# Performance work log

Measured on AMD Instinct MI355X. Metric: run time of the kernel, lower is better.

The kernel has to match this reference:

```python
import jax, jax.numpy as jnp
import numpy as np

THRESHOLD = 0.5
NEG_POS_RATIO = 3
ALPHA = 10.0
N_PRIORS = 8732
N_CLASSES = 21
BATCH = 128
N_OBJ = 32


def cxcy_to_xy(cxcy):
    return jnp.concatenate([cxcy[..., :2] - cxcy[..., 2:] / 2.0,
                            cxcy[..., :2] + cxcy[..., 2:] / 2.0], axis=-1)


def xy_to_cxcy(xy):
    return jnp.concatenate([(xy[..., :2] + xy[..., 2:]) / 2.0,
                            xy[..., 2:] - xy[..., :2]], axis=-1)


def cxcy_to_gcxgcy(cxcy, priors_cxcy):
    return jnp.concatenate([(cxcy[..., :2] - priors_cxcy[..., :2]) / (priors_cxcy[..., 2:] / 10.0),
                            jnp.log(cxcy[..., 2:] / priors_cxcy[..., 2:]) * 5.0], axis=-1)


def find_jaccard_overlap(a, b):
    # a: (M,4) xyxy, b: (P,4) xyxy -> (M,P)
    lt = jnp.maximum(a[:, None, :2], b[None, :, :2])
    rb = jnp.minimum(a[:, None, 2:], b[None, :, 2:])
    wh = jnp.clip(rb - lt, 0.0)
    inter = wh[..., 0] * wh[..., 1]
    area_a = (a[:, 2] - a[:, 0]) * (a[:, 3] - a[:, 1])
    area_b = (b[:, 2] - b[:, 0]) * (b[:, 3] - b[:, 1])
    return inter / (area_a[:, None] + area_b[None, :] - inter)


def _match_one(boxes, labels, priors_xy, priors_cxcy):
    # boxes: (M,4) xyxy, labels: (M,)
    iou = find_jaccard_overlap(boxes, priors_xy)           # (M,P)
    obj_idx = jnp.argmax(iou, axis=1)                      # best prior per object
    iou = iou.at[jnp.arange(boxes.shape[0]), obj_idx].set(1.0)
    positive = (iou >= THRESHOLD).any(axis=0)              # (P,)
    max_prior_idx = jnp.argmax(iou, axis=0)                # best object per prior
    true_cls = labels[max_prior_idx] * positive.astype(labels.dtype)
    matched = boxes[max_prior_idx]                         # (P,4)
    true_locs = cxcy_to_gcxgcy(xy_to_cxcy(matched), priors_cxcy)
    return true_locs, true_cls, positive


def setup_inputs() -> dict:
    key = jax.random.key(0)
    k1, k2, k3, k4, k5, k6 = jax.random.split(key, 6)
    pred_loc = jax.random.normal(k1, (BATCH, N_PRIORS, 4), dtype=jnp.float32)
    pred_cls = jax.random.normal(k2, (BATCH, N_PRIORS, N_CLASSES), dtype=jnp.float32)
    # valid xyxy gt boxes in [0,1]
    p1 = jax.random.uniform(k3, (BATCH, N_OBJ, 2))
    p2 = jax.random.uniform(k4, (BATCH, N_OBJ, 2))
    b_boxes = jnp.concatenate([jnp.minimum(p1, p2), jnp.maximum(p1, p2) + 1e-3], axis=-1)
    b_boxes = jnp.clip(b_boxes, 0.0, 1.0).astype(jnp.float32)
    b_labels = jax.random.randint(k5, (BATCH, N_OBJ), 1, N_CLASSES)
    cxy = jax.random.uniform(k6, (N_PRIORS, 2), minval=0.1, maxval=0.9)
    wh = jax.random.uniform(jax.random.fold_in(k6, 1), (N_PRIORS, 2), minval=0.05, maxval=0.3)
    priors_cxcy = jnp.concatenate([cxy, wh], axis=-1).astype(jnp.float32)
    return {"pred_loc": pred_loc, "pred_cls": pred_cls, "b_boxes": b_boxes,
            "b_labels": b_labels, "priors_cxcy": priors_cxcy}


def reference(pred_loc, pred_cls, b_boxes, b_labels, priors_cxcy):
    batch_size, n_priors, n_classes = pred_cls.shape
    priors_xy = cxcy_to_xy(priors_cxcy)
    true_locs, true_classes, positive = jax.vmap(
        _match_one, in_axes=(0, 0, None, None))(b_boxes, b_labels, priors_xy, priors_cxcy)
    pos_f = positive.astype(pred_loc.dtype)                 # (B,P)
    n_positives = positive.sum(axis=1)                      # (B,)
    n_pos_total = n_positives.sum().astype(pred_loc.dtype)
    # L1 loss (mean over positive box elements)
    loc_loss = (jnp.abs(pred_loc - true_locs) * pos_f[..., None]).sum() / (n_pos_total * 4.0)
    # per-prior cross-entropy
    logp = jax.nn.log_softmax(pred_cls, axis=-1)
    ce = -jnp.take_along_axis(logp, true_classes[..., None], axis=-1)[..., 0]  # (B,P)
    conf_loss_pos = (ce * pos_f).sum()
    # hard negative mining: sort negatives descending per image
    conf_neg = jnp.where(positive, 0.0, ce)
    conf_neg_sorted = -jnp.sort(-conf_neg, axis=1)
    ranks = jnp.arange(n_priors)[None, :]
    hard_mask = ranks < (NEG_POS_RATIO * n_positives)[:, None]
    conf_loss_hard_neg = jnp.where(hard_mask, conf_neg_sorted, 0.0).sum()
    conf_loss = (conf_loss_hard_neg + conf_loss_pos) / n_pos_total
    loc_loss = ALPHA * loc_loss
    total_loss = conf_loss + loc_loss
    return total_loss, loc_loss, conf_loss
```

## Files before the change

### kernel.cpp

```cpp
#include <hip/hip_runtime.h>
#include <math.h>

#define B 128
#define M 32
#define P 8732
#define C 21
#define ALPHA 10.0f
#define TPB2 256
#define PPT 2
#define PPB (TPB2 * PPT)
#define NB2 18
#define CH 8
#define CS 1092

__global__ __launch_bounds__(256) void k1_partial(
    const float* __restrict__ b_boxes, const float* __restrict__ priors,
    float* __restrict__ pI, float* __restrict__ pU, int* __restrict__ pidx,
    int* __restrict__ done) {
  if (blockIdx.x == 0 && threadIdx.x == 0) *done = 0;
  int b = blockIdx.x >> 3;
  int ch = blockIdx.x & 7;
  int wid = threadIdx.x >> 6;
  int lane = threadIdx.x & 63;
  int obase = wid * 8;

  float ox1[8], oy1[8], ox2[8], oy2[8], oarea[8], bI[8], bU[8];
  int bidx[8];
#pragma unroll
  for (int k = 0; k < 8; k++) {
    float4 bx = ((const float4*)b_boxes)[(size_t)b * M + obase + k];
    ox1[k] = bx.x; oy1[k] = bx.y; ox2[k] = bx.z; oy2[k] = bx.w;
    oarea[k] = (bx.z - bx.x) * (bx.w - bx.y);
    bI[k] = -1.0f; bU[k] = 1.0f; bidx[k] = P;
  }

  int pend = (ch + 1) * CS;
  if (pend > P) pend = P;
#pragma unroll 2
  for (int p = ch * CS + lane; p < pend; p += 64) {
    float4 pr = ((const float4*)priors)[p];
    float pw2 = pr.z * 0.5f, ph2 = pr.w * 0.5f;
    float px1 = pr.x - pw2, py1 = pr.y - ph2;
    float px2 = pr.x + pw2, py2 = pr.y + ph2;
    float areaP = pr.z * pr.w;
#pragma unroll
    for (int k = 0; k < 8; k++) {
      float iw = fminf(ox2[k], px2) - fmaxf(ox1[k], px1);
      float ih = fminf(oy2[k], py2) - fmaxf(oy1[k], py1);
      iw = fmaxf(iw, 0.0f);
      ih = fmaxf(ih, 0.0f);
      float inter = iw * ih;
      float uni = oarea[k] + areaP - inter;
      if (inter * bU[k] > bI[k] * uni) { bI[k] = inter; bU[k] = uni; bidx[k] = p; }
    }
  }
  for (int off = 32; off >= 1; off >>= 1) {
#pragma unroll
    for (int k = 0; k < 8; k++) {
      float oI = __shfl_xor(bI[k], off, 64);
      float oU = __shfl_xor(bU[k], off, 64);
      int oi = __shfl_xor(bidx[k], off, 64);
      float l = oI * bU[k], r = bI[k] * oU;
      if (l > r || (l == r && oi < bidx[k])) { bI[k] = oI; bU[k] = oU; bidx[k] = oi; }
    }
  }
  if (lane == 0) {
#pragma unroll
    for (int k = 0; k < 8; k++) {
      int idx = ((size_t)b * M + obase + k) * CH + ch;
      pI[idx] = bI[k]; pU[idx] = bU[k]; pidx[idx] = bidx[k];
    }
  }
}

__global__ __launch_bounds__(256) void k1_reduce(
    const float* __restrict__ pI, const float* __restrict__ pU,
    const int* __restrict__ pidx, int* __restrict__ objidx) {
  int o = blockIdx.x * 256 + threadIdx.x;
  if (o >= B * M) return;
  float cI = pI[o * CH], cU = pU[o * CH];
  int ci = pidx[o * CH];
#pragma unroll
  for (int ch = 1; ch < CH; ch++) {
    float nI = pI[o * CH + ch], nU = pU[o * CH + ch];
    int ni = pidx[o * CH + ch];
    if (nI * cU > cI * nU) { cI = nI; cU = nU; ci = ni; }
  }
  objidx[o] = ci;
}

__global__ __launch_bounds__(TPB2, 5) void k2_perprior(
    const float* __restrict__ pred_loc, const float* __restrict__ pred_cls,
    const float* __restrict__ b_boxes, const int* __restrict__ b_labels,
    const float* __restrict__ priors, const int* __restrict__ objidx,
    float* __restrict__ ploc, float* __restrict__ pce, int* __restrict__ pnp,
    float* __restrict__ confneg) {
  int b = blockIdx.y;
  int p0 = blockIdx.x * PPB;
  int tid = threadIdx.x;

  __shared__ float sx1[M], sy1[M], sx2[M], sy2[M], sarea[M];
  __shared__ int slab[M], sobj[M];
  __shared__ int sinv[PPB];
  if (tid < M) {
    int m = tid;
    float4 bx = ((const float4*)b_boxes)[b * M + m];
    sx1[m] = bx.x; sy1[m] = bx.y; sx2[m] = bx.z; sy2[m] = bx.w;
    sarea[m] = (bx.z - bx.x) * (bx.w - bx.y);
    slab[m] = b_labels[b * M + m];
    sobj[m] = objidx[b * M + m];
  }
  sinv[tid] = 0x7fffffff;
  sinv[tid + 256] = 0x7fffffff;
  __syncthreads();
  if (tid < M) {
    int t = sobj[tid] - p0;
    if (t >= 0 && t < PPB) atomicMin(&sinv[t], tid);
  }
  __syncthreads();

  float locpart = 0.0f, cepospart = 0.0f;
  int npos = 0;
  int pbase = p0 + tid * PPT;
  if (pbase < P) {
    float4 pr[PPT];
    pr[0] = ((const float4*)priors)[pbase];
    pr[1] = ((const float4*)priors)[pbase + 1];
    const float2* pc2 =
        (const float2*)(pred_cls + ((size_t)b * P + p0) * C) + 21 * tid;
    float2 q[21];
#pragma unroll
    for (int i = 0; i < 21; i++) q[i] = pc2[i];
    const float* u = (const float*)q;
    const float4* plp = (const float4*)pred_loc + (size_t)b * P + pbase;
    float4 pl[PPT];
    pl[0] = plp[0];
    pl[1] = plp[1];

    float px1[PPT], py1[PPT], px2[PPT], py2[PPT], areaP[PPT];
    float bI[PPT], bU[PPT];
    int bm[PPT];
#pragma unroll
    for (int j = 0; j < PPT; j++) {
      float pw2 = pr[j].z * 0.5f, ph2 = pr[j].w * 0.5f;
      px1[j] = pr[j].x - pw2; py1[j] = pr[j].y - ph2;
      px2[j] = pr[j].x + pw2; py2[j] = pr[j].y + ph2;
      areaP[j] = pr[j].z * pr[j].w;
      bI[j] = -1.0f; bU[j] = 1.0f; bm[j] = 0;
    }
    for (int m = 0; m < M; m++) {
      float bx1 = sx1[m], by1 = sy1[m], bx2 = sx2[m], by2 = sy2[m];
      float ar = sarea[m];
#pragma unroll
      for (int j = 0; j < PPT; j++) {
        float iw = fminf(bx2, px2[j]) - fmaxf(bx1, px1[j]);
        float ih = fminf(by2, py2[j]) - fmaxf(by1, py1[j]);
        iw = fmaxf(iw, 0.0f);
        ih = fmaxf(ih, 0.0f);
        float inter = iw * ih;
        float uni = ar + areaP[j] - inter;
        if (inter * bU[j] > bI[j] * uni) { bI[j] = inter; bU[j] = uni; bm[j] = m; }
      }
    }
    bool pos[PPT];
#pragma unroll
    for (int j = 0; j < PPT; j++) {
      int fm = sinv[tid * PPT + j];
      if (fm != 0x7fffffff) {
        if (!((bI[j] == bU[j]) && (bm[j] < fm))) {
          bI[j] = 1.0f; bU[j] = 1.0f; bm[j] = fm;
        }
      }
      pos[j] = (2.0f * bI[j] >= bU[j]);
    }
    int wAny = __any((int)(pos[0] | pos[1]));

    if (wAny) {
#pragma unroll
      for (int j = 0; j < PPT; j++) {
        int mj = bm[j];
        float bx1 = sx1[mj], by1 = sy1[mj], bx2 = sx2[mj], by2 = sy2[mj];
        float cx = (bx1 + bx2) * 0.5f, cy = (by1 + by2) * 0.5f;
        float w = bx2 - bx1, h = by2 - by1;
        float rz = __builtin_amdgcn_rcpf(pr[j].z);
        float rw = __builtin_amdgcn_rcpf(pr[j].w);
        float g0 = (cx - pr[j].x) * 10.0f * rz;
        float g1 = (cy - pr[j].y) * 10.0f * rw;
        float g2 = __logf(w * rz) * 5.0f;
        float g3 = __logf(h * rw) * 5.0f;
        if (pos[j]) {
          locpart += fabsf(pl[j].x - g0) + fabsf(pl[j].y - g1) +
                     fabsf(pl[j].z - g2) + fabsf(pl[j].w - g3);
          npos++;
        }
      }
    }

    float cn[PPT];
#pragma unroll
    for (int j = 0; j < PPT; j++) {
      float se = 0.0f;
#pragma unroll
      for (int c = 0; c < C; c++) se += __expf(u[j * C + c]);
      float lse = __logf(se);
      cn[j] = pos[j] ? 0.0f : (lse - u[j * C]);
      if (wAny) {
        int cls = pos[j] ? slab[bm[j]] : 0;
        float vc = u[j * C];
#pragma unroll
        for (int c = 1; c < C; c++)
          if (c == cls) vc = u[j * C + c];
        cepospart += pos[j] ? (lse - vc) : 0.0f;
      }
    }
    ((float2*)confneg)[((size_t)b * P + pbase) >> 1] = make_float2(cn[0], cn[1]);
  }

  for (int off = 32; off >= 1; off >>= 1) {
    locpart += __shfl_down(locpart, off, 64);
    cepospart += __shfl_down(cepospart, off, 64);
    npos += __shfl_down(npos, off, 64);
  }
  __shared__ float rloc[4], rce[4];
  __shared__ int rnp[4];
  int wid = tid >> 6;
  if ((tid & 63) == 0) { rloc[wid] = locpart; rce[wid] = cepospart; rnp[wid] = npos; }
  __syncthreads();
  if (tid == 0) {
    int f = b * NB2 + blockIdx.x;
    ploc[f] = rloc[0] + rloc[1] + rloc[2] + rloc[3];
    pce[f] = rce[0] + rce[1] + rce[2] + rce[3];
    pnp[f] = rnp[0] + rnp[1] + rnp[2] + rnp[3];
  }
}

__global__ __launch_bounds__(1024) void k3_hardneg(
    const float* __restrict__ confneg,
    const float* __restrict__ ploc, const float* __restrict__ pce,
    const int* __restrict__ pnp,
    float* __restrict__ imgres, int* __restrict__ done,
    float* __restrict__ out) {
  int b = blockIdx.x;
  int tid = threadIdx.x;
  int wid = tid >> 6;
  int lane = tid & 63;

  __shared__ __align__(16) float s[P];
  __shared__ int histw[16 * 256];
  __shared__ __align__(16) int cnt[256];
  __shared__ int sdig, scum, sK, sLast;
  __shared__ float sLoc, sCe, sNp;
  __shared__ float rsum[16], rl[16], rc[16], rh[16], rn[16];
  __shared__ int rcnt[16];

  {
    const float4* row4 = (const float4*)(confneg + (size_t)b * P);
    for (int i = tid; i < P / 4; i += 1024) ((float4*)s)[i] = row4[i];
  }

  if (wid == 0) {
    float lp = 0.0f, cp = 0.0f;
    int np = 0;
    if (lane < NB2) {
      int f = b * NB2 + lane;
      lp = ploc[f]; cp = pce[f]; np = pnp[f];
    }
    for (int off = 32; off >= 1; off >>= 1) {
      lp += __shfl_down(lp, off, 64);
      cp += __shfl_down(cp, off, 64);
      np += __shfl_down(np, off, 64);
    }
    if (lane == 0) {
      int K = np * 3;
      if (K > P) K = P;
      sK = K; sLoc = lp; sCe = cp; sNp = (float)np;
    }
  }
  __syncthreads();

  int K = sK;
  unsigned pfx = 0;
  int Krem = K;
#pragma unroll
  for (int pass = 3; pass >= 0; --pass) {
    int sh = pass * 8;
    for (int i = tid; i < 16 * 256; i += 1024) histw[i] = 0;
    __syncthreads();
    unsigned himask = (pass == 3) ? 0u : (0xFFFFFFFFu << (sh + 8));
    int* myh = &histw[wid * 256];
    for (int i = tid; i < P; i += 1024) {
      unsigned ub = __float_as_uint(s[i]);
      if ((ub & himask) == pfx) atomicAdd(&myh[(ub >> sh) & 255], 1);
    }
    __syncthreads();
    if (tid < 256) {
      int c = 0;
#pragma unroll
      for (int w = 0; w < 16; w++) c += histw[w * 256 + tid];
      cnt[tid] = c;
    }
    __syncthreads();
    if (wid == 0) {
      int4 c4 = ((const int4*)cnt)[lane];
      int s3 = c4.w;
      int s2 = c4.z + s3;
      int s1 = c4.y + s2;
      int s0 = c4.x + s1;
      int suf = s0;
      for (int off = 1; off < 64; off <<= 1) {
        int t = __shfl_down(suf, off, 64);
        if (lane + off < 64) suf += t;
      }
      int above = suf - s0;
      int S0 = above + s0, S1 = above + s1, S2 = above + s2, S3 = above + s3;
      int S4 = above;
      if (S3 >= Krem && S4 < Krem) { sdig = 4 * lane + 3; scum = S4; }
      else if (S2 >= Krem && S3 < Krem) { sdig = 4 * lane + 2; scum = S3; }
      else if (S1 >= Krem && S2 < Krem) { sdig = 4 * lane + 1; scum = S2; }
      else if (S0 >= Krem && S1 < Krem) { sdig = 4 * lane + 0; scum = S1; }
    }
    __syncthreads();
    pfx |= ((unsigned)sdig) << sh;
    Krem -= scum;
  }
  float tau = __uint_as_float(pfx);

  float sum = 0.0f;
  int cgt = 0;
  for (int i = tid; i < P; i += 1024) {
    float v = s[i];
    if (v > tau) { sum += v; cgt++; }
  }
  for (int off = 32; off >= 1; off >>= 1) {
    sum += __shfl_down(sum, off, 64);
    cgt += __shfl_down(cgt, off, 64);
  }
  if (lane == 0) { rsum[wid] = sum; rcnt[wid] = cgt; }
  __syncthreads();
  if (tid == 0) {
    float stot = 0.0f;
    int ctot = 0;
#pragma unroll
    for (int w = 0; w < 16; w++) { stot += rsum[w]; ctot += rcnt[w]; }
    float hard = stot + (float)(K - ctot) * tau;
    imgres[b * 4 + 0] = sLoc;
    imgres[b * 4 + 1] = sCe;
    imgres[b * 4 + 2] = hard;
    imgres[b * 4 + 3] = sNp;
    __threadfence();
    int prev = atomicAdd(done, 1);
    sLast = (prev == B - 1) ? 1 : 0;
  }
  __syncthreads();
  if (sLast) {
    __threadfence();
    float l = 0.0f, c = 0.0f, h = 0.0f, n = 0.0f;
    if (tid < B) {
      l = atomicAdd(&imgres[tid * 4 + 0], 0.0f);
      c = atomicAdd(&imgres[tid * 4 + 1], 0.0f);
      h = atomicAdd(&imgres[tid * 4 + 2], 0.0f);
      n = atomicAdd(&imgres[tid * 4 + 3], 0.0f);
    }
    for (int off = 32; off >= 1; off >>= 1) {
      l += __shfl_down(l, off, 64);
      c += __shfl_down(c, off, 64);
      h += __shfl_down(h, off, 64);
      n += __shfl_down(n, off, 64);
    }
    if (lane == 0) { rl[wid] = l; rc[wid] = c; rh[wid] = h; rn[wid] = n; }
    __syncthreads();
    if (tid == 0) {
      float L = 0, Cc = 0, H = 0, N = 0;
#pragma unroll
      for (int w = 0; w < 16; w++) { L += rl[w]; Cc += rc[w]; H += rh[w]; N += rn[w]; }
      float loc = ALPHA * L / (N * 4.0f);
      float conf = (H + Cc) / N;
      out[0] = conf + loc;
      out[1] = loc;
      out[2] = conf;
    }
  }
}

extern "C" void kernel_launch(void* const* d_in, const int* in_sizes, int n_in,
                              void* d_out, int out_size, void* d_ws, size_t ws_size,
                              hipStream_t stream) {
  (void)in_sizes; (void)n_in; (void)out_size; (void)ws_size;
  const float* pred_loc = (const float*)d_in[0];
  const float* pred_cls = (const float*)d_in[1];
  const float* b_boxes = (const float*)d_in[2];
  const int* b_labels = (const int*)d_in[3];
  const float* priors = (const float*)d_in[4];
  float* out = (float*)d_out;

  int* done = (int*)d_ws;
  float* ploc = (float*)d_ws + 8;
  float* pce = ploc + B * NB2;
  int* pnp = (int*)(pce + B * NB2);
  float* imgres = (float*)(pnp + B * NB2);
  float* pI = imgres + B * 4;
  float* pU = pI + B * M * CH;
  int* pidx = (int*)(pU + B * M * CH);
  int* objidx = pidx + B * M * CH;
  float* confneg = (float*)(objidx + B * M);

  k1_partial<<<B * CH, 256, 0, stream>>>(b_boxes, priors, pI, pU, pidx, done);
  k1_reduce<<<(B * M + 255) / 256, 256, 0, stream>>>(pI, pU, pidx, objidx);
  dim3 g2(NB2, B);
  k2_perprior<<<g2, TPB2, 0, stream>>>(pred_loc, pred_cls, b_boxes, b_labels,
                                       priors, objidx, ploc, pce, pnp, confneg);
  k3_hardneg<<<B, 1024, 0, stream>>>(confneg, ploc, pce, pnp, imgres, done, out);
}
```

Baseline: 221.6 us.

## Fold objidx reduction into per-prior kernel and stage class logits through LDS

```diff
diff --git a/kernel.cpp b/kernel.cpp
--- a/kernel.cpp
+++ b/kernel.cpp
@@ -7,9 +7,8 @@
 #define C 21
 #define ALPHA 10.0f
 #define TPB2 256
-#define PPT 2
-#define PPB (TPB2 * PPT)
-#define NB2 18
+#define PPB 256
+#define NB2 35
 #define CH 8
 #define CS 1092
 
@@ -73,147 +72,117 @@
   }
 }
 
-__global__ __launch_bounds__(256) void k1_reduce(
-    const float* __restrict__ pI, const float* __restrict__ pU,
-    const int* __restrict__ pidx, int* __restrict__ objidx) {
-  int o = blockIdx.x * 256 + threadIdx.x;
-  if (o >= B * M) return;
-  float cI = pI[o * CH], cU = pU[o * CH];
-  int ci = pidx[o * CH];
-#pragma unroll
-  for (int ch = 1; ch < CH; ch++) {
-    float nI = pI[o * CH + ch], nU = pU[o * CH + ch];
-    int ni = pidx[o * CH + ch];
-    if (nI * cU > cI * nU) { cI = nI; cU = nU; ci = ni; }
-  }
-  objidx[o] = ci;
-}
-
-__global__ __launch_bounds__(TPB2, 5) void k2_perprior(
+__global__ __launch_bounds__(TPB2) void k2_perprior(
     const float* __restrict__ pred_loc, const float* __restrict__ pred_cls,
     const float* __restrict__ b_boxes, const int* __restrict__ b_labels,
-    const float* __restrict__ priors, const int* __restrict__ objidx,
+    const float* __restrict__ priors,
+    const float* __restrict__ pI, const float* __restrict__ pU,
+    const int* __restrict__ pidx,
     float* __restrict__ ploc, float* __restrict__ pce, int* __restrict__ pnp,
     float* __restrict__ confneg) {
   int b = blockIdx.y;
   int p0 = blockIdx.x * PPB;
   int tid = threadIdx.x;
-
+  int wid = tid >> 6;
+  int lane = tid & 63;
+
+  __shared__ __align__(16) float sCls[4 * 64 * C];
   __shared__ float sx1[M], sy1[M], sx2[M], sy2[M], sarea[M];
   __shared__ int slab[M], sobj[M];
   __shared__ int sinv[PPB];
+
+  sinv[tid] = 0x7fffffff;
   if (tid < M) {
     int m = tid;
     float4 bx = ((const float4*)b_boxes)[b * M + m];
     sx1[m] = bx.x; sy1[m] = bx.y; sx2[m] = bx.z; sy2[m] = bx.w;
     sarea[m] = (bx.z - bx.x) * (bx.w - bx.y);
     slab[m] = b_labels[b * M + m];
-    sobj[m] = objidx[b * M + m];
-  }
-  sinv[tid] = 0x7fffffff;
-  sinv[tid + 256] = 0x7fffffff;
+    int o = b * M + m;
+    float cI = pI[o * CH], cU = pU[o * CH];
+    int ci = pidx[o * CH];
+#pragma unroll
+    for (int ch = 1; ch < CH; ch++) {
+      float nI = pI[o * CH + ch], nU = pU[o * CH + ch];
+      int ni = pidx[o * CH + ch];
+      if (nI * cU > cI * nU) { cI = nI; cU = nU; ci = ni; }
+    }
+    sobj[m] = ci;
+  }
   __syncthreads();
   if (tid < M) {
     int t = sobj[tid] - p0;
     if (t >= 0 && t < PPB) atomicMin(&sinv[t], tid);
   }
+  {
+    int wp0 = p0 + wid * 64;
+    int nv = P - wp0;
+    nv = nv < 0 ? 0 : (nv > 64 ? 64 : nv);
+    int nf4 = (nv * C) >> 2;
+    const float4* src = (const float4*)(pred_cls + ((size_t)b * P + wp0) * C);
+    float4* dst = (float4*)&sCls[wid * 64 * C];
+    for (int i = lane; i < nf4; i += 64) dst[i] = src[i];
+  }
   __syncthreads();
 
   float locpart = 0.0f, cepospart = 0.0f;
   int npos = 0;
-  int pbase = p0 + tid * PPT;
-  if (pbase < P) {
-    float4 pr[PPT];
-    pr[0] = ((const float4*)priors)[pbase];
-    pr[1] = ((const float4*)priors)[pbase + 1];
-    const float2* pc2 =
-        (const float2*)(pred_cls + ((size_t)b * P + p0) * C) + 21 * tid;
-    float2 q[21];
-#pragma unroll
-    for (int i = 0; i < 21; i++) q[i] = pc2[i];
-    const float* u = (const float*)q;
-    const float4* plp = (const float4*)pred_loc + (size_t)b * P + pbase;
-    float4 pl[PPT];
-    pl[0] = plp[0];
-    pl[1] = plp[1];
-
-    float px1[PPT], py1[PPT], px2[PPT], py2[PPT], areaP[PPT];
-    float bI[PPT], bU[PPT];
-    int bm[PPT];
-#pragma unroll
-    for (int j = 0; j < PPT; j++) {
-      float pw2 = pr[j].z * 0.5f, ph2 = pr[j].w * 0.5f;
-      px1[j] = pr[j].x - pw2; py1[j] = pr[j].y - ph2;
-      px2[j] = pr[j].x + pw2; py2[j] = pr[j].y + ph2;
-      areaP[j] = pr[j].z * pr[j].w;
-      bI[j] = -1.0f; bU[j] = 1.0f; bm[j] = 0;
-    }
+  int p = p0 + tid;
+  if (p < P) {
+    float4 pr = ((const float4*)priors)[p];
+    float pw2 = pr.z * 0.5f, ph2 = pr.w * 0.5f;
+    float px1 = pr.x - pw2, py1 = pr.y - ph2;
+    float px2 = pr.x + pw2, py2 = pr.y + ph2;
+    float areaP = pr.z * pr.w;
+    float bI = -1.0f, bU = 1.0f;
+    int bm = 0;
     for (int m = 0; m < M; m++) {
-      float bx1 = sx1[m], by1 = sy1[m], bx2 = sx2[m], by2 = sy2[m];
-      float ar = sarea[m];
-#pragma unroll
-      for (int j = 0; j < PPT; j++) {
-        float iw = fminf(bx2, px2[j]) - fmaxf(bx1, px1[j]);
-        float ih = fminf(by2, py2[j]) - fmaxf(by1, py1[j]);
-        iw = fmaxf(iw, 0.0f);
-        ih = fmaxf(ih, 0.0f);
-        float inter = iw * ih;
-        float uni = ar + areaP[j] - inter;
-        if (inter * bU[j] > bI[j] * uni) { bI[j] = inter; bU[j] = uni; bm[j] = m; }
+      float iw = fminf(sx2[m], px2) - fmaxf(sx1[m], px1);
+      float ih = fminf(sy2[m], py2) - fmaxf(sy1[m], py1);
+      iw = fmaxf(iw, 0.0f);
+      ih = fmaxf(ih, 0.0f);
+      float inter = iw * ih;
+      float uni = sarea[m] + areaP - inter;
+      if (inter * bU > bI * uni) { bI = inter; bU = uni; bm = m; }
+    }
+    int fm = sinv[tid];
+    if (fm != 0x7fffffff) {
+      if (!((bI == bU) && (bm < fm))) { bI = 1.0f; bU = 1.0f; bm = fm; }
+    }
+    bool pos = (2.0f * bI >= bU);
+    int wAny = __any((int)pos);
+
+    if (wAny) {
+      float4 pl = ((const float4*)pred_loc)[(size_t)b * P + p];
+      float bx1 = sx1[bm], by1 = sy1[bm], bx2 = sx2[bm], by2 = sy2[bm];
+      float cx = (bx1 + bx2) * 0.5f, cy = (by1 + by2) * 0.5f;
+      float w = bx2 - bx1, h = by2 - by1;
+      float rz = __builtin_amdgcn_rcpf(pr.z);
+      float rw = __builtin_amdgcn_rcpf(pr.w);
+      float g0 = (cx - pr.x) * 10.0f * rz;
+      float g1 = (cy - pr.y) * 10.0f * rw;
+      float g2 = __logf(w * rz) * 5.0f;
+      float g3 = __logf(h * rw) * 5.0f;
+      if (pos) {
+        locpart = fabsf(pl.x - g0) + fabsf(pl.y - g1) +
+                  fabsf(pl.z - g2) + fabsf(pl.w - g3);
+        npos = 1;
       }
     }
-    bool pos[PPT];
-#pragma unroll
-    for (int j = 0; j < PPT; j++) {
-      int fm = sinv[tid * PPT + j];
-      if (fm != 0x7fffffff) {
-        if (!((bI[j] == bU[j]) && (bm[j] < fm))) {
-          bI[j] = 1.0f; bU[j] = 1.0f; bm[j] = fm;
-        }
-      }
-      pos[j] = (2.0f * bI[j] >= bU[j]);
-    }
-    int wAny = __any((int)(pos[0] | pos[1]));
-
-    if (wAny) {
-#pragma unroll
-      for (int j = 0; j < PPT; j++) {
-        int mj = bm[j];
-        float bx1 = sx1[mj], by1 = sy1[mj], bx2 = sx2[mj], by2 = sy2[mj];
-        float cx = (bx1 + bx2) * 0.5f, cy = (by1 + by2) * 0.5f;
-        float w = bx2 - bx1, h = by2 - by1;
-        float rz = __builtin_amdgcn_rcpf(pr[j].z);
-        float rw = __builtin_amdgcn_rcpf(pr[j].w);
-        float g0 = (cx - pr[j].x) * 10.0f * rz;
-        float g1 = (cy - pr[j].y) * 10.0f * rw;
-        float g2 = __logf(w * rz) * 5.0f;
-        float g3 = __logf(h * rw) * 5.0f;
-        if (pos[j]) {
-          locpart += fabsf(pl[j].x - g0) + fabsf(pl[j].y - g1) +
-                     fabsf(pl[j].z - g2) + fabsf(pl[j].w - g3);
-          npos++;
-        }
-      }
-    }
-
-    float cn[PPT];
-#pragma unroll
-    for (int j = 0; j < PPT; j++) {
-      float se = 0.0f;
-#pragma unroll
-      for (int c = 0; c < C; c++) se += __expf(u[j * C + c]);
-      float lse = __logf(se);
-      cn[j] = pos[j] ? 0.0f : (lse - u[j * C]);
-      if (wAny) {
-        int cls = pos[j] ? slab[bm[j]] : 0;
-        float vc = u[j * C];
-#pragma unroll
-        for (int c = 1; c < C; c++)
-          if (c == cls) vc = u[j * C + c];
-        cepospart += pos[j] ? (lse - vc) : 0.0f;
-      }
-    }
-    ((float2*)confneg)[((size_t)b * P + pbase) >> 1] = make_float2(cn[0], cn[1]);
+
+    const float* u = &sCls[(wid * 64 + lane) * C];
+    int cls = pos ? slab[bm] : 0;
+    float se = 0.0f, vc = 0.0f;
+#pragma unroll
+    for (int c = 0; c < C; c++) {
+      float x = u[c];
+      se += __expf(x);
+      if (c == cls) vc = x;
+    }
+    float lse = __logf(se);
+    float ce = lse - vc;
+    confneg[(size_t)b * P + p] = pos ? 0.0f : ce;
+    cepospart = pos ? ce : 0.0f;
   }
 
   for (int off = 32; off >= 1; off >>= 1) {
@@ -223,8 +192,7 @@
   }
   __shared__ float rloc[4], rce[4];
   __shared__ int rnp[4];
-  int wid = tid >> 6;
-  if ((tid & 63) == 0) { rloc[wid] = locpart; rce[wid] = cepospart; rnp[wid] = npos; }
+  if (lane == 0) { rloc[wid] = locpart; rce[wid] = cepospart; rnp[wid] = npos; }
   __syncthreads();
   if (tid == 0) {
     int f = b * NB2 + blockIdx.x;
@@ -401,13 +369,12 @@
   float* pI = imgres + B * 4;
   float* pU = pI + B * M * CH;
   int* pidx = (int*)(pU + B * M * CH);
-  int* objidx = pidx + B * M * CH;
-  float* confneg = (float*)(objidx + B * M);
+  float* confneg = (float*)(pidx + B * M * CH);
 
   k1_partial<<<B * CH, 256, 0, stream>>>(b_boxes, priors, pI, pU, pidx, done);
-  k1_reduce<<<(B * M + 255) / 256, 256, 0, stream>>>(pI, pU, pidx, objidx);
   dim3 g2(NB2, B);
   k2_perprior<<<g2, TPB2, 0, stream>>>(pred_loc, pred_cls, b_boxes, b_labels,
-                                       priors, objidx, ploc, pce, pnp, confneg);
+                                       priors, pI, pU, pidx,
+                                       ploc, pce, pnp, confneg);
   k3_hardneg<<<B, 1024, 0, stream>>>(confneg, ploc, pce, pnp, imgres, done, out);
 }
```

After: 221.6 us. Within noise of the previous version (+0.0%).
